# Kernel tuning notes

Measured on AMD Instinct MI355X. Metric: run time of the kernel, lower is better.

Reference implementation:

```python
import jax, jax.numpy as jnp
import numpy as np
from jax import lax

K = 40
EPS = 1e-5
SLOPE = 0.2


def knn_idx(x, k):
    # x: (B, C, N); returns (B, N, k) indices of k nearest (L2), self included
    xx = jnp.sum(x * x, axis=1)                      # (B, N)
    inner = jnp.einsum('bcn,bcm->bnm', x, x)         # (B, N, N)
    dist = xx[:, :, None] - 2.0 * inner + xx[:, None, :]
    _, idx = lax.top_k(-dist, k)
    return idx


def get_graph_feature(x, k):
    # x: (B, C, N) -> (B, 2C, N, k)
    idx = knn_idx(x, k)
    xt = jnp.transpose(x, (0, 2, 1))                 # (B, N, C)
    feat = jax.vmap(lambda t, i: t[i])(xt, idx)      # (B, N, k, C)
    center = xt[:, :, None, :]                       # (B, N, 1, C)
    e = jnp.concatenate([feat - center, jnp.broadcast_to(center, feat.shape)], axis=-1)
    return jnp.transpose(e, (0, 3, 1, 2))            # (B, 2C, N, k)


def edge_block(x, W, gamma, beta, k):
    # EdgeConv: graph feature -> 1x1 conv -> BN(train-mode) -> LeakyReLU -> max over k
    e = get_graph_feature(x, k)                      # (B, 2C, N, k)
    y = jnp.einsum('oc,bcnk->bonk', W, e)            # (B, 32, N, k)
    m = jnp.mean(y, axis=(0, 2, 3), keepdims=True)
    v = jnp.mean((y - m) ** 2, axis=(0, 2, 3), keepdims=True)
    y = (y - m) / jnp.sqrt(v + EPS)
    y = y * gamma[None, :, None, None] + beta[None, :, None, None]
    y = jnp.where(y >= 0, y, SLOPE * y)
    return jnp.max(y, axis=-1)                       # (B, 32, N)


def setup_inputs() -> dict:
    key = jax.random.key(0)
    ks = jax.random.split(key, 16)
    B, C, N = 8, 9, 2048
    d = {
        'x': jax.random.normal(ks[0], (B, C, N), jnp.float32),
        'W1': jax.random.normal(ks[1], (32, 18), jnp.float32) * 0.1,
        'W2': jax.random.normal(ks[2], (32, 64), jnp.float32) * 0.1,
        'W3': jax.random.normal(ks[3], (32, 64), jnp.float32) * 0.1,
        'W4': jax.random.normal(ks[4], (32, 64), jnp.float32) * 0.1,
        'W5': jax.random.normal(ks[5], (128, 128), jnp.float32) * 0.1,
    }
    for i in range(4):
        d[f'g{i+1}'] = jnp.ones((32,), jnp.float32)
        d[f'b{i+1}'] = jnp.zeros((32,), jnp.float32)
    return d


def reference(x, W1, W2, W3, W4, W5, g1, g2, g3, g4, b1, b2, b3, b4):
    x1 = edge_block(x, W1, g1, b1, K)
    x2 = edge_block(x1, W2, g2, b2, K) + x1
    x3 = edge_block(x2, W3, g3, b3, K) + x2
    x4 = edge_block(x3, W4, g4, b4, K) + x3
    cat = jnp.concatenate([x1, x2, x3, x4], axis=1)  # (B, 128, N)
    return jnp.einsum('oc,bcn->bon', W5, cat)        # (B, 128, N)
```

## Files before the change

kernel.cpp:

```cpp
#include <hip/hip_runtime.h>
#include <stdint.h>

#define NP 2048
#define KNN 40
#define CAP 128

__device__ __forceinline__ unsigned fOrd(float f) {
    unsigned u = __float_as_uint(f);
    return u ^ ((unsigned)((int)u >> 31) | 0x80000000u);
}
__device__ __forceinline__ unsigned long long dOrd(double d) {
    unsigned long long u = (unsigned long long)__double_as_longlong(d);
    return u ^ (((unsigned long long)((long long)u >> 63)) | 0x8000000000000000ull);
}

template<int C, int CP, int CPX>
__global__ void prep_kernel(const float* __restrict__ X, long bstride,
                            const float* __restrict__ W,
                            float* __restrict__ p, float* __restrict__ r,
                            float* __restrict__ xx, float* __restrict__ XT) {
    __shared__ float wdT[C][32];
    __shared__ float wrT[C][32];
    int tid = threadIdx.x;
    for (int i = tid; i < 32 * C; i += 256) {
        int o = i / C, c = i - o * C;
        float wd = W[o * 2 * C + c];
        float wc = W[o * 2 * C + C + c];
        wdT[c][o] = wd;
        wrT[c][o] = wc - wd;
    }
    __syncthreads();
    int lane = tid & 63;
    int o = lane & 31;
    int h = lane >> 5;
    int wv = tid >> 6;
    int flat = blockIdx.x * 8 + wv * 2 + h;
    int b = flat >> 11, n = flat & 2047;
    const float* Xb = X + (long)b * bstride + n;
    float pacc = 0.f, racc = 0.f, xxa = 0.f, xto = 0.f;
    double xxd = 0.0;
#pragma unroll
    for (int c = 0; c < C; c++) {
        float xv = Xb[(long)c * NP];
        pacc = fmaf(wdT[c][o], xv, pacc);
        racc = fmaf(wrT[c][o], xv, racc);
        xxa += xv * xv;
        xxd += (double)xv * (double)xv;
        if (c == o) xto = xv;
    }
    long base = ((long)b * NP + n) * 32 + o;
    p[base] = pacc;
    r[base] = racc;
    long rowb = ((long)b * NP + n) * CPX;
    if (o < CP) XT[rowb + o] = (o < C) ? xto : 0.f;
    if (o == 0) {
        xx[b * NP + n] = xxa;
        *reinterpret_cast<double*>(&XT[rowb + CP]) = xxd;
    }
}

template<int C, int CP, int CPX>
__global__ __launch_bounds__(512, 2)
void knn_kernel(const float* __restrict__ X, long bstride,
                const float* __restrict__ p, const float* __restrict__ r,
                const float* __restrict__ xx, const float* __restrict__ XT,
                float* __restrict__ mmax, float* __restrict__ mmin,
                float* __restrict__ sums) {
    constexpr int XT_FLOATS = 2 * C * 128;
    constexpr int CS_FLOATS = 16 * CAP + 16 * KNN;
    constexpr int UNI_FLOATS = (XT_FLOATS > CS_FLOATS) ? XT_FLOATS : CS_FLOATS;
    __shared__ __align__(16) float uni[UNI_FLOATS];
    __shared__ __align__(16) float xxt[256];
    __shared__ __align__(8) float qld[8][CP][2];
    __shared__ float S1loc[32], S2loc[32];
    int* candb = (int*)uni;
    int* selb  = (int*)uni + 16 * CAP;
    int tid = threadIdx.x;
    if (tid < 32) { S1loc[tid] = 0.f; S2loc[tid] = 0.f; }
    int lane = tid & 63;
    int wv = tid >> 6;
    int half = lane >> 5;
    int l32 = lane & 31;
    int b = blockIdx.x >> 7;
    int n0 = (blockIdx.x & 127) * 16;
    int nA = n0 + wv * 2, nB = nA + 1;
    int rowA = wv * 2, rowB = rowA + 1;
    const float* Xb = X + (long)b * bstride;
    const float* XTb = XT + (long)b * NP * CPX;
    long bNP = (long)b * NP;

    if (lane < CP) {
        qld[wv][lane][0] = XTb[(long)nA * CPX + lane];
        qld[wv][lane][1] = XTb[(long)nB * CPX + lane];
    }
    float xxnA = xx[bNP + nA];
    float xxnB = xx[bNP + nB];

    unsigned uA[16], uB[16];
    for (int t2 = 0; t2 < 8; t2++) {
        __syncthreads();
        for (int i = tid; i < C * 64; i += 512) {
            int c = i >> 6, g = i & 63;
            int tt = g >> 5, gg = g & 31;
            *(float4*)&uni[tt * (C * 128) + c * 128 + gg * 4] =
                *(const float4*)&Xb[(long)c * NP + (t2 * 2 + tt) * 128 + gg * 4];
        }
        if (tid < 256) xxt[tid] = xx[bNP + t2 * 256 + tid];
        __syncthreads();
        const float* xth = uni + half * (C * 128);
        float4 ia = make_float4(0.f, 0.f, 0.f, 0.f);
        float4 ib = make_float4(0.f, 0.f, 0.f, 0.f);
#pragma unroll
        for (int c = 0; c < C; c++) {
            float2 q = *(const float2*)&qld[wv][c][0];
            float4 xv = *(const float4*)&xth[c * 128 + 4 * l32];
            ia.x = fmaf(q.x, xv.x, ia.x);
            ia.y = fmaf(q.x, xv.y, ia.y);
            ia.z = fmaf(q.x, xv.z, ia.z);
            ia.w = fmaf(q.x, xv.w, ia.w);
            ib.x = fmaf(q.y, xv.x, ib.x);
            ib.y = fmaf(q.y, xv.y, ib.y);
            ib.z = fmaf(q.y, xv.z, ib.z);
            ib.w = fmaf(q.y, xv.w, ib.w);
        }
        float4 xm = *(const float4*)&xxt[half * 128 + 4 * l32];
        unsigned a0 = fOrd((xxnA - 2.0f * ia.x) + xm.x) >> 16;
        unsigned a1 = fOrd((xxnA - 2.0f * ia.y) + xm.y) >> 16;
        unsigned a2 = fOrd((xxnA - 2.0f * ia.z) + xm.z) >> 16;
        unsigned a3 = fOrd((xxnA - 2.0f * ia.w) + xm.w) >> 16;
        unsigned b0 = fOrd((xxnB - 2.0f * ib.x) + xm.x) >> 16;
        unsigned b1 = fOrd((xxnB - 2.0f * ib.y) + xm.y) >> 16;
        unsigned b2_ = fOrd((xxnB - 2.0f * ib.z) + xm.z) >> 16;
        unsigned b3 = fOrd((xxnB - 2.0f * ib.w) + xm.w) >> 16;
        uA[2 * t2]     = (a1 << 16) | a0;
        uA[2 * t2 + 1] = (a3 << 16) | a2;
        uB[2 * t2]     = (b1 << 16) | b0;
        uB[2 * t2 + 1] = (b3 << 16) | b2_;
    }
    __syncthreads();

    unsigned long long lmlt = (1ull << lane) - 1ull;

    double xxdA = *reinterpret_cast<const double*>(&XTb[(long)nA * CPX + CP]);
    double xxdB = *reinterpret_cast<const double*>(&XTb[(long)nB * CPX + CP]);

    unsigned vA = 0u, vB = 0u;
    for (int bit = 15; bit >= 0; bit--) {
        unsigned tA = vA | ((1u << bit) - 1u);
        unsigned tB = vB | ((1u << bit) - 1u);
        int cA = 0, cB = 0;
#pragma unroll
        for (int t = 0; t < 16; t++) {
            cA += __popcll(__ballot((uA[t] & 0xFFFFu) <= tA));
            cA += __popcll(__ballot((uA[t] >> 16) <= tA));
            cB += __popcll(__ballot((uB[t] & 0xFFFFu) <= tB));
            cB += __popcll(__ballot((uB[t] >> 16) <= tB));
        }
        if (cA < KNN) vA |= (1u << bit);
        if (cB < KNN) vB |= (1u << bit);
    }
    unsigned thrA = (vA > 0xFFFEu) ? 0xFFFFu : vA + 1u;
    unsigned thrB = (vB > 0xFFFEu) ? 0xFFFFu : vB + 1u;

    int baseA = 0, baseB = 0;
#pragma unroll
    for (int kk = 0; kk < 16; kk++) {
#pragma unroll
        for (int hh = 0; hh < 2; hh++) {
            unsigned kA = hh ? (uA[kk] >> 16) : (uA[kk] & 0xFFFFu);
            unsigned kB = hh ? (uB[kk] >> 16) : (uB[kk] & 0xFFFFu);
            int idx = (kk >> 1) * 256 + half * 128 + 4 * l32 + (kk & 1) * 2 + hh;
            bool pA = (kA <= thrA), pB = (kB <= thrB);
            unsigned long long mkA = __ballot(pA), mkB = __ballot(pB);
            if (pA) {
                int pos = baseA + __popcll(mkA & lmlt);
                if (pos < CAP) candb[rowA * CAP + pos] = idx;
            }
            if (pB) {
                int pos = baseB + __popcll(mkB & lmlt);
                if (pos < CAP) candb[rowB * CAP + pos] = idx;
            }
            baseA += __popcll(mkA);
            baseB += __popcll(mkB);
        }
    }
    int cntA = baseA < CAP ? baseA : CAP;
    int cntB = baseB < CAP ? baseB : CAP;

    unsigned long long keyA[CAP / 64], keyB[CAP / 64];
    int mixA[CAP / 64], mixB[CAP / 64];
#pragma unroll
    for (int s3 = 0; s3 < CAP / 64; s3++) {
        int slot = s3 * 64 + lane;
        keyA[s3] = ~0ull; mixA[s3] = 0;
        keyB[s3] = ~0ull; mixB[s3] = 0;
        if (slot < cntA) {
            int m = candb[rowA * CAP + slot] & (NP - 1);
            mixA[s3] = m;
            const float* xmp = XTb + (long)m * CPX;
            double inner = 0.0;
#pragma unroll
            for (int g = 0; g < CP / 4; g++) {
                float4 v = *(const float4*)&xmp[g * 4];
                inner += (double)qld[wv][g * 4 + 0][0] * (double)v.x;
                inner += (double)qld[wv][g * 4 + 1][0] * (double)v.y;
                inner += (double)qld[wv][g * 4 + 2][0] * (double)v.z;
                inner += (double)qld[wv][g * 4 + 3][0] * (double)v.w;
            }
            double xxm = *reinterpret_cast<const double*>(&xmp[CP]);
            double dd = (xxdA - 2.0 * inner) + xxm;
            keyA[s3] = dOrd(dd);
        }
        if (slot < cntB) {
            int m = candb[rowB * CAP + slot] & (NP - 1);
            mixB[s3] = m;
            const float* xmp = XTb + (long)m * CPX;
            double inner = 0.0;
#pragma unroll
            for (int g = 0; g < CP / 4; g++) {
                float4 v = *(const float4*)&xmp[g * 4];
                inner += (double)qld[wv][g * 4 + 0][1] * (double)v.x;
                inner += (double)qld[wv][g * 4 + 1][1] * (double)v.y;
                inner += (double)qld[wv][g * 4 + 2][1] * (double)v.z;
                inner += (double)qld[wv][g * 4 + 3][1] * (double)v.w;
            }
            double xxm = *reinterpret_cast<const double*>(&xmp[CP]);
            double dd = (xxdB - 2.0 * inner) + xxm;
            keyB[s3] = dOrd(dd);
        }
    }

    auto cex = [](unsigned long long& k, int& i, const int S, const bool keepmin) {
        unsigned long long pk = __shfl_xor(k, S);
        int pi = __shfl_xor(i, S);
        bool less = (k < pk) || (k == pk && i < pi);
        bool tp = (less != keepmin);
        k = tp ? pk : k;
        i = tp ? pi : i;
    };
    if (cntA <= 64 && cntB <= 64) {
#pragma unroll
        for (int kk2 = 1; kk2 <= 6; kk2++) {
            const int K = 1 << kk2;
#pragma unroll
            for (int ss = kk2 - 1; ss >= 0; ss--) {
                const int S = 1 << ss;
                bool asc0 = (K == 64) ? true : ((lane & K) == 0);
                bool km0 = ((lane & S) == 0) == asc0;
                cex(keyA[0], mixA[0], S, km0);
                cex(keyB[0], mixB[0], S, km0);
            }
        }
    } else {
#pragma unroll
        for (int kk2 = 1; kk2 <= 6; kk2++) {
            const int K = 1 << kk2;
#pragma unroll
            for (int ss = kk2 - 1; ss >= 0; ss--) {
                const int S = 1 << ss;
                bool ascL = (lane & K) == 0;
                bool asc0 = (K == 64) ? true  : ascL;
                bool asc1 = (K == 64) ? false : ascL;
                bool km0 = ((lane & S) == 0) == asc0;
                bool km1 = ((lane & S) == 0) == asc1;
                cex(keyA[0], mixA[0], S, km0);
                cex(keyA[1], mixA[1], S, km1);
                cex(keyB[0], mixB[0], S, km0);
                cex(keyB[1], mixB[1], S, km1);
            }
        }
        {
            bool lA = (keyA[0] < keyA[1]) || (keyA[0] == keyA[1] && mixA[0] < mixA[1]);
            unsigned long long tk = keyA[0]; int ti = mixA[0];
            keyA[0] = lA ? keyA[0] : keyA[1];  mixA[0] = lA ? mixA[0] : mixA[1];
            keyA[1] = lA ? keyA[1] : tk;       mixA[1] = lA ? mixA[1] : ti;
            bool lB = (keyB[0] < keyB[1]) || (keyB[0] == keyB[1] && mixB[0] < mixB[1]);
            tk = keyB[0]; ti = mixB[0];
            keyB[0] = lB ? keyB[0] : keyB[1];  mixB[0] = lB ? mixB[0] : mixB[1];
            keyB[1] = lB ? keyB[1] : tk;       mixB[1] = lB ? mixB[1] : ti;
        }
#pragma unroll
        for (int ss = 5; ss >= 0; ss--) {
            const int S = 1 << ss;
            bool km = ((lane & S) == 0);
            cex(keyA[0], mixA[0], S, km);
            cex(keyA[1], mixA[1], S, km);
            cex(keyB[0], mixB[0], S, km);
            cex(keyB[1], mixB[1], S, km);
        }
    }
    if (lane < KNN) {
        selb[rowA * KNN + lane] = mixA[0];
        selb[rowB * KNN + lane] = mixB[0];
    }

    {
        int o = lane & 31, h = lane >> 5;
        float s1A = 0.f, s2A = 0.f, s1B = 0.f, s2B = 0.f;
        float mxA = -__builtin_inff(), mnA = __builtin_inff();
        float mxB = -__builtin_inff(), mnB = __builtin_inff();
        const float* pb = p + bNP * 32 + o;
        for (int k = h * 20; k < h * 20 + 20; k++) {
            int mA = selb[rowA * KNN + k] & (NP - 1);
            int mB = selb[rowB * KNN + k] & (NP - 1);
            float pvA = pb[(long)mA * 32];
            float pvB = pb[(long)mB * 32];
            s1A += pvA;
            s2A = fmaf(pvA, pvA, s2A);
            mxA = fmaxf(mxA, pvA);
            mnA = fminf(mnA, pvA);
            s1B += pvB;
            s2B = fmaf(pvB, pvB, s2B);
            mxB = fmaxf(mxB, pvB);
            mnB = fminf(mnB, pvB);
        }
        s1A += __shfl_xor(s1A, 32);
        s2A += __shfl_xor(s2A, 32);
        mxA = fmaxf(mxA, __shfl_xor(mxA, 32));
        mnA = fminf(mnA, __shfl_xor(mnA, 32));
        s1B += __shfl_xor(s1B, 32);
        s2B += __shfl_xor(s2B, 32);
        mxB = fmaxf(mxB, __shfl_xor(mxB, 32));
        mnB = fminf(mnB, __shfl_xor(mnB, 32));
        if (h == 0) {
            long bseA = (bNP + nA) * 32 + o;
            float qA = r[bseA];
            mmax[bseA] = mxA + qA;
            mmin[bseA] = mnA + qA;
            atomicAdd(&S1loc[o], s1A + 40.f * qA);
            atomicAdd(&S2loc[o], fmaf(2.f * qA, s1A, fmaf(40.f * qA, qA, s2A)));
            long bseB = (bNP + nB) * 32 + o;
            float qB = r[bseB];
            mmax[bseB] = mxB + qB;
            mmin[bseB] = mnB + qB;
            atomicAdd(&S1loc[o], s1B + 40.f * qB);
            atomicAdd(&S2loc[o], fmaf(2.f * qB, s1B, fmaf(40.f * qB, qB, s2B)));
        }
    }
    __syncthreads();
    if (tid < 32) {
        atomicAdd(&sums[tid], S1loc[tid]);
        atomicAdd(&sums[32 + tid], S2loc[tid]);
    }
}

__global__ void finish_kernel(const float* __restrict__ mmax, const float* __restrict__ mmin,
                              const float* __restrict__ sums,
                              const float* __restrict__ g, const float* __restrict__ be,
                              const float* __restrict__ resid,
                              float* __restrict__ outb) {
    int id = blockIdx.x * 256 + threadIdx.x;
    int b = id >> 16;
    int o = (id >> 11) & 31;
    int n = id & 2047;
    const float cntf = 655360.0f;
    float mean = sums[o] / cntf;
    float var = sums[32 + o] / cntf - mean * mean;
    float sc = g[o] / sqrtf(var + 1e-5f);
    float sh = be[o] - mean * sc;
    long bse = ((long)b * NP + n) * 32 + o;
    float v = (sc >= 0.f) ? mmax[bse] : mmin[bse];
    float y = sc * v + sh;
    y = (y >= 0.f) ? y : 0.2f * y;
    long ob = ((long)b * 128 + o) * NP + n;
    if (resid) y += resid[ob];
    outb[ob] = y;
}

__global__ void final_gemm(const float* __restrict__ W5, float* __restrict__ out) {
    __shared__ __align__(16) float catL[128][32];
    int b = blockIdx.x >> 6;
    int n0 = (blockIdx.x & 63) * 32;
    int tid = threadIdx.x;
    for (int i = tid; i < 128 * 32; i += 256) {
        int c = i >> 5, nn = i & 31;
        catL[c][nn] = out[((long)b * 128 + c) * NP + n0 + nn];
    }
    __syncthreads();
    int og = tid >> 3, ng = tid & 7;
    int o0 = og * 4, nl = ng * 4;
    float acc[4][4] = {};
    for (int c = 0; c < 128; c++) {
        float4 cv = *(const float4*)&catL[c][nl];
#pragma unroll
        for (int i = 0; i < 4; i++) {
            float w = W5[(o0 + i) * 128 + c];
            acc[i][0] = fmaf(w, cv.x, acc[i][0]);
            acc[i][1] = fmaf(w, cv.y, acc[i][1]);
            acc[i][2] = fmaf(w, cv.z, acc[i][2]);
            acc[i][3] = fmaf(w, cv.w, acc[i][3]);
        }
    }
#pragma unroll
    for (int i = 0; i < 4; i++) {
        float4 vv = make_float4(acc[i][0], acc[i][1], acc[i][2], acc[i][3]);
        *(float4*)&out[((long)b * 128 + o0 + i) * NP + n0 + nl] = vv;
    }
}

extern "C" void kernel_launch(void* const* d_in, const int* in_sizes, int n_in,
                              void* d_out, int out_size, void* d_ws, size_t ws_size,
                              hipStream_t stream) {
    const float* x  = (const float*)d_in[0];
    const float* W1 = (const float*)d_in[1];
    const float* W2 = (const float*)d_in[2];
    const float* W3 = (const float*)d_in[3];
    const float* W4 = (const float*)d_in[4];
    const float* W5 = (const float*)d_in[5];
    const float* g1 = (const float*)d_in[6];
    const float* b1 = (const float*)d_in[7];
    const float* g2 = (const float*)d_in[8];
    const float* b2 = (const float*)d_in[9];
    const float* g3 = (const float*)d_in[10];
    const float* b3 = (const float*)d_in[11];
    const float* g4 = (const float*)d_in[12];
    const float* b4 = (const float*)d_in[13];
    float* out = (float*)d_out;
    float* ws  = (float*)d_ws;
    float* p    = ws;
    float* r    = ws + 524288;
    float* mmax = ws + 1048576;
    float* mmin = ws + 1572864;
    float* xx   = ws + 2097152;
    float* sums = ws + 2113536;
    float* XT   = ws + 2113792;
    hipMemsetAsync(sums, 0, 256 * sizeof(float), stream);

    prep_kernel<9, 12, 16><<<2048, 256, 0, stream>>>(x, 9L * NP, W1, p, r, xx, XT);
    knn_kernel<9, 12, 16><<<1024, 512, 0, stream>>>(x, 9L * NP, p, r, xx, XT, mmax, mmin, sums);
    finish_kernel<<<2048, 256, 0, stream>>>(mmax, mmin, sums, g1, b1, nullptr, out);
    const float* x1 = out;
    prep_kernel<32, 32, 36><<<2048, 256, 0, stream>>>(x1, 128L * NP, W2, p, r, xx, XT);
    knn_kernel<32, 32, 36><<<1024, 512, 0, stream>>>(x1, 128L * NP, p, r, xx, XT, mmax, mmin, sums + 64);
    finish_kernel<<<2048, 256, 0, stream>>>(mmax, mmin, sums + 64, g2, b2, x1, out + 32 * NP);
    const float* x2 = out + 32 * NP;
    prep_kernel<32, 32, 36><<<2048, 256, 0, stream>>>(x2, 128L * NP, W3, p, r, xx, XT);
    knn_kernel<32, 32, 36><<<1024, 512, 0, stream>>>(x2, 128L * NP, p, r, xx, XT, mmax, mmin, sums + 128);
    finish_kernel<<<2048, 256, 0, stream>>>(mmax, mmin, sums + 128, g3, b3, x2, out + 64 * NP);
    const float* x3 = out + 64 * NP;
    prep_kernel<32, 32, 36><<<2048, 256, 0, stream>>>(x3, 128L * NP, W4, p, r, xx, XT);
    knn_kernel<32, 32, 36><<<1024, 512, 0, stream>>>(x3, 128L * NP, p, r, xx, XT, mmax, mmin, sums + 192);
    finish_kernel<<<2048, 256, 0, stream>>>(mmax, mmin, sums + 192, g4, b4, x3, out + 96 * NP);

    final_gemm<<<512, 256, 0, stream>>>(W5, out);
}
```

Baseline: 605.0 us.

## Double-buffer point tiles with register prefetch in kNN distance loop

```diff
diff --git a/kernel.cpp b/kernel.cpp
--- a/kernel.cpp
+++ b/kernel.cpp
@@ -66,11 +66,13 @@
                 const float* __restrict__ xx, const float* __restrict__ XT,
                 float* __restrict__ mmax, float* __restrict__ mmin,
                 float* __restrict__ sums) {
-    constexpr int XT_FLOATS = 2 * C * 128;
+    constexpr int TILE_F = C * 128;
+    constexpr int NF4 = C * 32;
+    constexpr int NIT = (NF4 + 511) / 512;
     constexpr int CS_FLOATS = 16 * CAP + 16 * KNN;
-    constexpr int UNI_FLOATS = (XT_FLOATS > CS_FLOATS) ? XT_FLOATS : CS_FLOATS;
+    constexpr int UNI_FLOATS = (2 * TILE_F > CS_FLOATS) ? 2 * TILE_F : CS_FLOATS;
     __shared__ __align__(16) float uni[UNI_FLOATS];
-    __shared__ __align__(16) float xxt[256];
+    __shared__ __align__(16) float xxl[NP];
     __shared__ __align__(8) float qld[8][CP][2];
     __shared__ float S1loc[32], S2loc[32];
     int* candb = (int*)uni;
@@ -79,8 +81,6 @@
     if (tid < 32) { S1loc[tid] = 0.f; S2loc[tid] = 0.f; }
     int lane = tid & 63;
     int wv = tid >> 6;
-    int half = lane >> 5;
-    int l32 = lane & 31;
     int b = blockIdx.x >> 7;
     int n0 = (blockIdx.x & 127) * 16;
     int nA = n0 + wv * 2, nB = nA + 1;
@@ -93,50 +93,55 @@
         qld[wv][lane][0] = XTb[(long)nA * CPX + lane];
         qld[wv][lane][1] = XTb[(long)nB * CPX + lane];
     }
+    for (int i = tid; i < NP; i += 512) xxl[i] = xx[bNP + i];
     float xxnA = xx[bNP + nA];
     float xxnB = xx[bNP + nB];
 
+    float4 sr0, sr1;
+#define STAGE_LOAD(tt) do {                                                    \
+        int i0_ = tid;                                                         \
+        if (NF4 == 1024 || i0_ < NF4)                                          \
+            sr0 = *(const float4*)&Xb[(long)(i0_ >> 5) * NP + (tt) * 128 + (i0_ & 31) * 4]; \
+        if (NIT > 1) {                                                         \
+            int i1_ = tid + 512;                                               \
+            sr1 = *(const float4*)&Xb[(long)(i1_ >> 5) * NP + (tt) * 128 + (i1_ & 31) * 4]; \
+        }                                                                      \
+    } while (0)
+
     unsigned uA[16], uB[16];
-    for (int t2 = 0; t2 < 8; t2++) {
+    STAGE_LOAD(0);
+    for (int t = 0; t < 16; t++) {
+        float* buf = uni + (t & 1) * TILE_F;
         __syncthreads();
-        for (int i = tid; i < C * 64; i += 512) {
-            int c = i >> 6, g = i & 63;
-            int tt = g >> 5, gg = g & 31;
-            *(float4*)&uni[tt * (C * 128) + c * 128 + gg * 4] =
-                *(const float4*)&Xb[(long)c * NP + (t2 * 2 + tt) * 128 + gg * 4];
-        }
-        if (tid < 256) xxt[tid] = xx[bNP + t2 * 256 + tid];
-        __syncthreads();
-        const float* xth = uni + half * (C * 128);
-        float4 ia = make_float4(0.f, 0.f, 0.f, 0.f);
-        float4 ib = make_float4(0.f, 0.f, 0.f, 0.f);
+        {
+            int i0 = tid;
+            if (NF4 == 1024 || i0 < NF4) *(float4*)&buf[i0 * 4] = sr0;
+            if (NIT > 1) { int i1 = tid + 512; *(float4*)&buf[i1 * 4] = sr1; }
+        }
+        if (t < 15) STAGE_LOAD(t + 1);
+        asm volatile("s_waitcnt lgkmcnt(0)" ::: "memory");
+        __builtin_amdgcn_s_barrier();
+        __builtin_amdgcn_sched_barrier(0);
+        float2 ia = make_float2(0.f, 0.f);
+        float2 ib = make_float2(0.f, 0.f);
 #pragma unroll
         for (int c = 0; c < C; c++) {
             float2 q = *(const float2*)&qld[wv][c][0];
-            float4 xv = *(const float4*)&xth[c * 128 + 4 * l32];
+            float2 xv = *(const float2*)&buf[c * 128 + 2 * lane];
             ia.x = fmaf(q.x, xv.x, ia.x);
             ia.y = fmaf(q.x, xv.y, ia.y);
-            ia.z = fmaf(q.x, xv.z, ia.z);
-            ia.w = fmaf(q.x, xv.w, ia.w);
             ib.x = fmaf(q.y, xv.x, ib.x);
             ib.y = fmaf(q.y, xv.y, ib.y);
-            ib.z = fmaf(q.y, xv.z, ib.z);
-            ib.w = fmaf(q.y, xv.w, ib.w);
-        }
-        float4 xm = *(const float4*)&xxt[half * 128 + 4 * l32];
+        }
+        float2 xm = *(const float2*)&xxl[t * 128 + 2 * lane];
         unsigned a0 = fOrd((xxnA - 2.0f * ia.x) + xm.x) >> 16;
         unsigned a1 = fOrd((xxnA - 2.0f * ia.y) + xm.y) >> 16;
-        unsigned a2 = fOrd((xxnA - 2.0f * ia.z) + xm.z) >> 16;
-        unsigned a3 = fOrd((xxnA - 2.0f * ia.w) + xm.w) >> 16;
         unsigned b0 = fOrd((xxnB - 2.0f * ib.x) + xm.x) >> 16;
         unsigned b1 = fOrd((xxnB - 2.0f * ib.y) + xm.y) >> 16;
-        unsigned b2_ = fOrd((xxnB - 2.0f * ib.z) + xm.z) >> 16;
-        unsigned b3 = fOrd((xxnB - 2.0f * ib.w) + xm.w) >> 16;
-        uA[2 * t2]     = (a1 << 16) | a0;
-        uA[2 * t2 + 1] = (a3 << 16) | a2;
-        uB[2 * t2]     = (b1 << 16) | b0;
-        uB[2 * t2 + 1] = (b3 << 16) | b2_;
-    }
+        uA[t] = (a1 << 16) | a0;
+        uB[t] = (b1 << 16) | b0;
+    }
+#undef STAGE_LOAD
     __syncthreads();
 
     unsigned long long lmlt = (1ull << lane) - 1ull;
@@ -169,7 +174,7 @@
         for (int hh = 0; hh < 2; hh++) {
             unsigned kA = hh ? (uA[kk] >> 16) : (uA[kk] & 0xFFFFu);
             unsigned kB = hh ? (uB[kk] >> 16) : (uB[kk] & 0xFFFFu);
-            int idx = (kk >> 1) * 256 + half * 128 + 4 * l32 + (kk & 1) * 2 + hh;
+            int idx = kk * 128 + 2 * lane + hh;
             bool pA = (kA <= thrA), pB = (kB <= thrB);
             unsigned long long mkA = __ballot(pA), mkB = __ballot(pB);
             if (pA) {
```

Result: slower. 648.9 us (+7.3%).

## Fuse BN finish into next layer prep and into final GEMM

Applied to the files above, without the earlier changes.

```diff
diff --git a/kernel.cpp b/kernel.cpp
--- a/kernel.cpp
+++ b/kernel.cpp
@@ -344,37 +344,112 @@
     }
 }
 
-__global__ void finish_kernel(const float* __restrict__ mmax, const float* __restrict__ mmin,
-                              const float* __restrict__ sums,
-                              const float* __restrict__ g, const float* __restrict__ be,
-                              const float* __restrict__ resid,
-                              float* __restrict__ outb) {
-    int id = blockIdx.x * 256 + threadIdx.x;
-    int b = id >> 16;
-    int o = (id >> 11) & 31;
-    int n = id & 2047;
+__global__ __launch_bounds__(256)
+void fp_kernel(const float* __restrict__ mmax, const float* __restrict__ mmin,
+               const float* __restrict__ sums_prev,
+               const float* __restrict__ g, const float* __restrict__ be,
+               const float* __restrict__ resid, float* __restrict__ outb,
+               const float* __restrict__ W,
+               float* __restrict__ p, float* __restrict__ r,
+               float* __restrict__ xx, float* __restrict__ XT) {
+    constexpr int C = 32, CP = 32, CPX = 36;
+    __shared__ float wdT[C][32];
+    __shared__ float wrT[C][32];
+    __shared__ float yb[8][33];
+    int tid = threadIdx.x;
+    for (int i = tid; i < 32 * C; i += 256) {
+        int o = i / C, c = i - o * C;
+        float wd = W[o * 2 * C + c];
+        float wc = W[o * 2 * C + C + c];
+        wdT[c][o] = wd;
+        wrT[c][o] = wc - wd;
+    }
+    int flat0 = blockIdx.x * 8;
+    int b = flat0 >> 11;
+    int nb = flat0 & 2047;
+    long bNP = (long)b * NP;
     const float cntf = 655360.0f;
-    float mean = sums[o] / cntf;
-    float var = sums[32 + o] / cntf - mean * mean;
-    float sc = g[o] / sqrtf(var + 1e-5f);
-    float sh = be[o] - mean * sc;
-    long bse = ((long)b * NP + n) * 32 + o;
-    float v = (sc >= 0.f) ? mmax[bse] : mmin[bse];
-    float y = sc * v + sh;
-    y = (y >= 0.f) ? y : 0.2f * y;
-    long ob = ((long)b * 128 + o) * NP + n;
-    if (resid) y += resid[ob];
-    outb[ob] = y;
-}
-
-__global__ void final_gemm(const float* __restrict__ W5, float* __restrict__ out) {
+    {
+        int pi = tid >> 5, c = tid & 31;
+        int n = nb + pi;
+        float mean = sums_prev[c] / cntf;
+        float var = sums_prev[32 + c] / cntf - mean * mean;
+        float sc = g[c] / sqrtf(var + 1e-5f);
+        float sh = be[c] - mean * sc;
+        long bse = (bNP + n) * 32 + c;
+        float v = (sc >= 0.f) ? mmax[bse] : mmin[bse];
+        float y = sc * v + sh;
+        y = (y >= 0.f) ? y : 0.2f * y;
+        yb[pi][c] = y;
+    }
+    __syncthreads();
+    {
+        int c = tid >> 3, ni = tid & 7;
+        int n = nb + ni;
+        long ob = ((long)b * 128 + c) * NP + n;
+        float y = yb[ni][c];
+        if (resid) y += resid[ob];
+        outb[ob] = y;
+        yb[ni][c] = y;
+    }
+    __syncthreads();
+    int lane = tid & 63;
+    int o = lane & 31;
+    int h = lane >> 5;
+    int wv = tid >> 6;
+    int pt = wv * 2 + h;
+    int n = nb + pt;
+    float pacc = 0.f, racc = 0.f, xxa = 0.f, xto = 0.f;
+    double xxd = 0.0;
+#pragma unroll
+    for (int c = 0; c < C; c++) {
+        float xv = yb[pt][c];
+        pacc = fmaf(wdT[c][o], xv, pacc);
+        racc = fmaf(wrT[c][o], xv, racc);
+        xxa += xv * xv;
+        xxd += (double)xv * (double)xv;
+        if (c == o) xto = xv;
+    }
+    long base = (bNP + n) * 32 + o;
+    p[base] = pacc;
+    r[base] = racc;
+    long rowb = (bNP + n) * CPX;
+    XT[rowb + o] = xto;
+    if (o == 0) {
+        xx[bNP + n] = xxa;
+        *reinterpret_cast<double*>(&XT[rowb + CP]) = xxd;
+    }
+}
+
+__global__ void final_gemm(const float* __restrict__ W5, float* __restrict__ out,
+                           const float* __restrict__ mmax, const float* __restrict__ mmin,
+                           const float* __restrict__ sums4,
+                           const float* __restrict__ g4, const float* __restrict__ be4) {
     __shared__ __align__(16) float catL[128][32];
     int b = blockIdx.x >> 6;
     int n0 = (blockIdx.x & 63) * 32;
     int tid = threadIdx.x;
+    const float cntf = 655360.0f;
+    long bNP = (long)b * NP;
     for (int i = tid; i < 128 * 32; i += 256) {
         int c = i >> 5, nn = i & 31;
-        catL[c][nn] = out[((long)b * 128 + c) * NP + n0 + nn];
+        float val;
+        if (c < 96) {
+            val = out[((long)b * 128 + c) * NP + n0 + nn];
+        } else {
+            int o = c - 96;
+            float mean = sums4[o] / cntf;
+            float var = sums4[32 + o] / cntf - mean * mean;
+            float sc = g4[o] / sqrtf(var + 1e-5f);
+            float sh = be4[o] - mean * sc;
+            long bse = (bNP + n0 + nn) * 32 + o;
+            float v = (sc >= 0.f) ? mmax[bse] : mmin[bse];
+            float y = sc * v + sh;
+            y = (y >= 0.f) ? y : 0.2f * y;
+            y += out[((long)b * 128 + 64 + o) * NP + n0 + nn];
+            val = y;
+        }
+        catL[c][nn] = val;
     }
     __syncthreads();
     int og = tid >> 3, ng = tid & 7;
@@ -428,19 +503,11 @@
 
     prep_kernel<9, 12, 16><<<2048, 256, 0, stream>>>(x, 9L * NP, W1, p, r, xx, XT);
     knn_kernel<9, 12, 16><<<1024, 512, 0, stream>>>(x, 9L * NP, p, r, xx, XT, mmax, mmin, sums);
-    finish_kernel<<<2048, 256, 0, stream>>>(mmax, mmin, sums, g1, b1, nullptr, out);
-    const float* x1 = out;
-    prep_kernel<32, 32, 36><<<2048, 256, 0, stream>>>(x1, 128L * NP, W2, p, r, xx, XT);
-    knn_kernel<32, 32, 36><<<1024, 512, 0, stream>>>(x1, 128L * NP, p, r, xx, XT, mmax, mmin, sums + 64);
-    finish_kernel<<<2048, 256, 0, stream>>>(mmax, mmin, sums + 64, g2, b2, x1, out + 32 * NP);
-    const float* x2 = out + 32 * NP;
-    prep_kernel<32, 32, 36><<<2048, 256, 0, stream>>>(x2, 128L * NP, W3, p, r, xx, XT);
-    knn_kernel<32, 32, 36><<<1024, 512, 0, stream>>>(x2, 128L * NP, p, r, xx, XT, mmax, mmin, sums + 128);
-    finish_kernel<<<2048, 256, 0, stream>>>(mmax, mmin, sums + 128, g3, b3, x2, out + 64 * NP);
-    const float* x3 = out + 64 * NP;
-    prep_kernel<32, 32, 36><<<2048, 256, 0, stream>>>(x3, 128L * NP, W4, p, r, xx, XT);
-    knn_kernel<32, 32, 36><<<1024, 512, 0, stream>>>(x3, 128L * NP, p, r, xx, XT, mmax, mmin, sums + 192);
-    finish_kernel<<<2048, 256, 0, stream>>>(mmax, mmin, sums + 192, g4, b4, x3, out + 96 * NP);
-
-    final_gemm<<<512, 256, 0, stream>>>(W5, out);
-}
+    fp_kernel<<<2048, 256, 0, stream>>>(mmax, mmin, sums, g1, b1, nullptr, out, W2, p, r, xx, XT);
+    knn_kernel<32, 32, 36><<<1024, 512, 0, stream>>>(out, 128L * NP, p, r, xx, XT, mmax, mmin, sums + 64);
+    fp_kernel<<<2048, 256, 0, stream>>>(mmax, mmin, sums + 64, g2, b2, out, out + 32 * NP, W3, p, r, xx, XT);
+    knn_kernel<32, 32, 36><<<1024, 512, 0, stream>>>(out + 32 * NP, 128L * NP, p, r, xx, XT, mmax, mmin, sums + 128);
+    fp_kernel<<<2048, 256, 0, stream>>>(mmax, mmin, sums + 128, g3, b3, out + 32 * NP, out + 64 * NP, W4, p, r, xx, XT);
+    knn_kernel<32, 32, 36><<<1024, 512, 0, stream>>>(out + 64 * NP, 128L * NP, p, r, xx, XT, mmax, mmin, sums + 192);
+    final_gemm<<<512, 256, 0, stream>>>(W5, out, mmax, mmin, sums + 192, g4, b4);
+}
```

Measured after the change: 591.5 us, median of 2. 2.2% less time.
